# Kernel tuning notes

Measured on AMD Instinct MI355X. Metric: run time of the kernel, lower is better.

## Reference

```python
import jax, jax.numpy as jnp
import numpy as np

B, T, C = 4, 2048, 2048
D_ATT, D_FFN = 2048, 8192
EPS = 1e-5

def setup_inputs() -> dict:
    key = jax.random.key(0)
    ks = jax.random.split(key, 20)
    n = lambda k, s, sc=0.02: jax.random.normal(k, s, dtype=jnp.float32) * sc
    u = lambda k, s: jax.random.uniform(k, s, dtype=jnp.float32)
    return {
        'x': jax.random.normal(ks[0], (B, T, C), dtype=jnp.float32),
        'ln1_w': jnp.ones((C,), jnp.float32), 'ln1_b': jnp.zeros((C,), jnp.float32),
        'ln2_w': jnp.ones((C,), jnp.float32), 'ln2_b': jnp.zeros((C,), jnp.float32),
        'tm_k': u(ks[1], (1, 1, C)), 'tm_v': u(ks[2], (1, 1, C)), 'tm_r': u(ks[3], (1, 1, C)),
        'time_decay': n(ks[4], (D_ATT,), 1.0),            # raw; decay = -exp(time_decay)
        'time_first': n(ks[5], (D_ATT,), 0.3) + float(np.log(0.3)),
        'Wk': n(ks[6], (D_ATT, C)), 'Wv': n(ks[7], (D_ATT, C)),
        'Wr': n(ks[8], (D_ATT, C)), 'Wo': n(ks[9], (C, D_ATT)),
        'cm_k': u(ks[10], (1, 1, C)), 'cm_r': u(ks[11], (1, 1, C)),
        'Wck': n(ks[12], (D_FFN, C)), 'Wcv': n(ks[13], (C, D_FFN)), 'Wcr': n(ks[14], (C, C)),
    }

def layer_norm(x, w, b):
    mu = jnp.mean(x, axis=-1, keepdims=True)
    var = jnp.var(x, axis=-1, keepdims=True)
    return (x - mu) * jax.lax.rsqrt(var + EPS) * w + b

def time_shift(x):
    # xx[:, t] = x[:, t-1], zero at t=0
    return jnp.pad(x, ((0, 0), (1, 0), (0, 0)))[:, :-1]

def wkv(time_decay, time_first, k, v):
    # Numerically-stable WKV linear recurrence (RWKV-4). k, v: [B,T,D]
    decay = -jnp.exp(time_decay)  # [D]
    kT = jnp.swapaxes(k, 0, 1)    # [T,B,D]
    vT = jnp.swapaxes(v, 0, 1)

    def step(carry, kv_t):
        aa, bb, pp = carry
        kt, vt = kv_t
        ww = time_first + kt
        p = jnp.maximum(pp, ww)
        e1 = jnp.exp(pp - p)
        e2 = jnp.exp(ww - p)
        out = (e1 * aa + e2 * vt) / (e1 * bb + e2)
        ww2 = pp + decay
        p2 = jnp.maximum(ww2, kt)
        e1b = jnp.exp(ww2 - p2)
        e2b = jnp.exp(kt - p2)
        return (e1b * aa + e2b * vt, e1b * bb + e2b, p2), out

    z = jnp.zeros((k.shape[0], k.shape[2]), k.dtype)
    init = (z, z, jnp.full_like(z, -1e38))
    _, outT = jax.lax.scan(step, init, (kT, vT))
    return jnp.swapaxes(outT, 0, 1)  # [B,T,D]

def reference(x, ln1_w, ln1_b, ln2_w, ln2_b, tm_k, tm_v, tm_r,
              time_decay, time_first, Wk, Wv, Wr, Wo,
              cm_k, cm_r, Wck, Wcv, Wcr):
    # --- TimeMix ---
    h = layer_norm(x, ln1_w, ln1_b)
    hh = time_shift(h)
    xk = h * tm_k + hh * (1 - tm_k)
    xv = h * tm_v + hh * (1 - tm_v)
    xr = h * tm_r + hh * (1 - tm_r)
    k = jnp.einsum('btc,dc->btd', xk, Wk)
    v = jnp.einsum('btc,dc->btd', xv, Wv)
    sr = jax.nn.sigmoid(jnp.einsum('btc,dc->btd', xr, Wr))
    rwkv = sr * wkv(time_decay, time_first, k, v)
    x = x + jnp.einsum('btd,cd->btc', rwkv, Wo)
    # --- ChannelMix ---
    g = layer_norm(x, ln2_w, ln2_b)
    gg = time_shift(g)
    xk2 = g * cm_k + gg * (1 - cm_k)
    xr2 = g * cm_r + gg * (1 - cm_r)
    kf = jnp.square(jax.nn.relu(jnp.einsum('btc,fc->btf', xk2, Wck)))
    kv = jnp.einsum('btf,cf->btc', kf, Wcv)
    x = x + jax.nn.sigmoid(jnp.einsum('btc,dc->btd', xr2, Wcr)) * kv
    return x
```

## Files before the change

kernel.cpp:

```cpp
#include <hip/hip_runtime.h>
#include <hip/hip_bf16.h>

#define B_ 4
#define T_ 2048
#define C_ 2048
#define D_ 2048
#define F_ 8192
#define BT_ (B_*T_)
#define NCH 64
#define LCH 32

using bf16 = __hip_bfloat16;
typedef __attribute__((ext_vector_type(8))) short bf16x8;
typedef __attribute__((ext_vector_type(4))) float f32x4;

template<bool V> struct BC { static constexpr bool value = V; };

struct bf4 { bf16 a, b, c, d; };

__device__ __forceinline__ bf4 to_bf4(float x, float y, float z, float w) {
  bf4 r;
  r.a = __float2bfloat16(x); r.b = __float2bfloat16(y);
  r.c = __float2bfloat16(z); r.d = __float2bfloat16(w);
  return r;
}

__device__ __forceinline__ void cvt_body(const float* __restrict__ in,
                                         bf16* __restrict__ out,
                                         int i, int stride, int n4) {
  for (; i < n4; i += stride) {
    float4 v = ((const float4*)in)[i];
    ((bf4*)out)[i] = to_bf4(v.x, v.y, v.z, v.w);
  }
}

__device__ __forceinline__ void block_reduce4(float v[4], float out[4]) {
  #pragma unroll
  for (int i = 0; i < 4; ++i)
    #pragma unroll
    for (int off = 1; off < 64; off <<= 1)
      v[i] += __shfl_xor(v[i], off);
  __shared__ float red[4][4];
  int wave = threadIdx.x >> 6, lane = threadIdx.x & 63;
  if (lane == 0) {
    red[wave][0] = v[0]; red[wave][1] = v[1];
    red[wave][2] = v[2]; red[wave][3] = v[3];
  }
  __syncthreads();
  #pragma unroll
  for (int i = 0; i < 4; ++i)
    out[i] = red[0][i] + red[1][i] + red[2][i] + red[3][i];
}

__global__ __launch_bounds__(256) void mixcvt1_kernel(
    const float* __restrict__ x, const float* __restrict__ w, const float* __restrict__ b,
    const float* __restrict__ tmk, const float* __restrict__ tmv, const float* __restrict__ tmr,
    bf16* __restrict__ xk, bf16* __restrict__ xv, bf16* __restrict__ xr,
    const float* __restrict__ W0, const float* __restrict__ W1,
    const float* __restrict__ W2, const float* __restrict__ W3,
    bf16* __restrict__ o0, bf16* __restrict__ o1,
    bf16* __restrict__ o2, bf16* __restrict__ o3) {
  if (blockIdx.x >= BT_) {
    const int lb4 = blockIdx.x - BT_;
    const int sub = lb4 >> 10;
    const int lb = lb4 & 1023;
    const float* in = (sub == 0) ? W0 : (sub == 1) ? W1 : (sub == 2) ? W2 : W3;
    bf16* o = (sub == 0) ? o0 : (sub == 1) ? o1 : (sub == 2) ? o2 : o3;
    cvt_body(in, o, lb * 256 + threadIdx.x, 1024 * 256, D_ * C_ / 4);
    return;
  }
  const int row = blockIdx.x;
  const int t = row & (T_ - 1);
  const bool hasPrev = (t != 0);
  const int tid = threadIdx.x;
  const float* xc = x + (size_t)row * C_;
  const float* xp = xc - C_;
  float c[8], p[8];
  *(float4*)&c[0] = *(const float4*)(xc + tid * 4);
  *(float4*)&c[4] = *(const float4*)(xc + tid * 4 + 1024);
  if (hasPrev) {
    *(float4*)&p[0] = *(const float4*)(xp + tid * 4);
    *(float4*)&p[4] = *(const float4*)(xp + tid * 4 + 1024);
  } else {
    #pragma unroll
    for (int j = 0; j < 8; ++j) p[j] = 0.f;
  }
  float v[4] = {0.f, 0.f, 0.f, 0.f}, tot[4];
  #pragma unroll
  for (int j = 0; j < 8; ++j) {
    v[0] += c[j]; v[1] += c[j] * c[j];
    v[2] += p[j]; v[3] += p[j] * p[j];
  }
  block_reduce4(v, tot);
  const float muc = tot[0] * (1.f / C_);
  const float rsc = rsqrtf(tot[1] * (1.f / C_) - muc * muc + 1e-5f);
  const float mup = tot[2] * (1.f / C_);
  const float rsp = rsqrtf(tot[3] * (1.f / C_) - mup * mup + 1e-5f);
  float wv[8], bv[8], mk[8], mv[8], mr[8];
  #pragma unroll
  for (int half = 0; half < 2; ++half) {
    int i = tid * 4 + half * 1024;
    *(float4*)&wv[half*4] = *(const float4*)(w + i);
    *(float4*)&bv[half*4] = *(const float4*)(b + i);
    *(float4*)&mk[half*4] = *(const float4*)(tmk + i);
    *(float4*)&mv[half*4] = *(const float4*)(tmv + i);
    *(float4*)&mr[half*4] = *(const float4*)(tmr + i);
  }
  float ok[8], ov[8], orr[8];
  #pragma unroll
  for (int j = 0; j < 8; ++j) {
    float h  = (c[j] - muc) * rsc * wv[j] + bv[j];
    float hh = hasPrev ? ((p[j] - mup) * rsp * wv[j] + bv[j]) : 0.f;
    ok[j]  = hh + mk[j] * (h - hh);
    ov[j]  = hh + mv[j] * (h - hh);
    orr[j] = hh + mr[j] * (h - hh);
  }
  size_t ro = (size_t)row * C_;
  #pragma unroll
  for (int half = 0; half < 2; ++half) {
    int i = tid * 4 + half * 1024;
    *(bf4*)(xk + ro + i) = to_bf4(ok[half*4], ok[half*4+1], ok[half*4+2], ok[half*4+3]);
    *(bf4*)(xv + ro + i) = to_bf4(ov[half*4], ov[half*4+1], ov[half*4+2], ov[half*4+3]);
    *(bf4*)(xr + ro + i) = to_bf4(orr[half*4], orr[half*4+1], orr[half*4+2], orr[half*4+3]);
  }
}

__global__ __launch_bounds__(256) void mixcvt2_kernel(
    const float* __restrict__ x, const float* __restrict__ w, const float* __restrict__ b,
    const float* __restrict__ cmk, const float* __restrict__ cmr,
    bf16* __restrict__ xk2, bf16* __restrict__ xr2,
    const float* __restrict__ Wcr, bf16* __restrict__ Wcr_b,
    const float* __restrict__ Wck, bf16* __restrict__ Wck_b) {
  if (blockIdx.x >= BT_) {
    const int lb = blockIdx.x - BT_;
    if (lb < 512)
      cvt_body(Wcr, Wcr_b, lb * 256 + threadIdx.x, 512 * 256, C_ * C_ / 4);
    else
      cvt_body(Wck, Wck_b, (lb - 512) * 256 + threadIdx.x, 2048 * 256, F_ * C_ / 4);
    return;
  }
  const int row = blockIdx.x;
  const int t = row & (T_ - 1);
  const bool hasPrev = (t != 0);
  const int tid = threadIdx.x;
  const float* xc = x + (size_t)row * C_;
  const float* xp = xc - C_;
  float c[8], p[8];
  *(float4*)&c[0] = *(const float4*)(xc + tid * 4);
  *(float4*)&c[4] = *(const float4*)(xc + tid * 4 + 1024);
  if (hasPrev) {
    *(float4*)&p[0] = *(const float4*)(xp + tid * 4);
    *(float4*)&p[4] = *(const float4*)(xp + tid * 4 + 1024);
  } else {
    #pragma unroll
    for (int j = 0; j < 8; ++j) p[j] = 0.f;
  }
  float v[4] = {0.f, 0.f, 0.f, 0.f}, tot[4];
  #pragma unroll
  for (int j = 0; j < 8; ++j) {
    v[0] += c[j]; v[1] += c[j] * c[j];
    v[2] += p[j]; v[3] += p[j] * p[j];
  }
  block_reduce4(v, tot);
  const float muc = tot[0] * (1.f / C_);
  const float rsc = rsqrtf(tot[1] * (1.f / C_) - muc * muc + 1e-5f);
  const float mup = tot[2] * (1.f / C_);
  const float rsp = rsqrtf(tot[3] * (1.f / C_) - mup * mup + 1e-5f);
  float wv[8], bv[8], mk[8], mr[8];
  #pragma unroll
  for (int half = 0; half < 2; ++half) {
    int i = tid * 4 + half * 1024;
    *(float4*)&wv[half*4] = *(const float4*)(w + i);
    *(float4*)&bv[half*4] = *(const float4*)(b + i);
    *(float4*)&mk[half*4] = *(const float4*)(cmk + i);
    *(float4*)&mr[half*4] = *(const float4*)(cmr + i);
  }
  float ok[8], orr[8];
  #pragma unroll
  for (int j = 0; j < 8; ++j) {
    float h  = (c[j] - muc) * rsc * wv[j] + bv[j];
    float hh = hasPrev ? ((p[j] - mup) * rsp * wv[j] + bv[j]) : 0.f;
    ok[j]  = hh + mk[j] * (h - hh);
    orr[j] = hh + mr[j] * (h - hh);
  }
  size_t ro = (size_t)row * C_;
  #pragma unroll
  for (int half = 0; half < 2; ++half) {
    int i = tid * 4 + half * 1024;
    *(bf4*)(xk2 + ro + i) = to_bf4(ok[half*4], ok[half*4+1], ok[half*4+2], ok[half*4+3]);
    *(bf4*)(xr2 + ro + i) = to_bf4(orr[half*4], orr[half*4+1], orr[half*4+2], orr[half*4+3]);
  }
}

__global__ __launch_bounds__(256) void wkv_pass1(
    const bf16* __restrict__ kp, const bf16* __restrict__ vp,
    const float* __restrict__ td,
    float* __restrict__ sA, float* __restrict__ sB, float* __restrict__ sP) {
  const int g = blockIdx.x * 256 + threadIdx.x;
  const int d = g & (D_ - 1);
  const int c = (g >> 11) & (NCH - 1);
  const int b = g >> 17;
  const float w = -__expf(td[d]);
  const size_t base = ((size_t)b * T_ + c * LCH) * D_ + d;
  float aa = 0.f, bb = 0.f, pp = -1e38f;
  #pragma unroll 4
  for (int j = 0; j < LCH; ++j) {
    float kt = __bfloat162float(kp[base + (size_t)j * D_]);
    float vt = __bfloat162float(vp[base + (size_t)j * D_]);
    float ww2 = pp + w;
    float p2 = fmaxf(ww2, kt);
    float e1 = __expf(ww2 - p2), e2 = __expf(kt - p2);
    aa = e1 * aa + e2 * vt;
    bb = e1 * bb + e2;
    pp = p2;
  }
  const int sidx = ((b * NCH + c) << 11) + d;
  sA[sidx] = aa; sB[sidx] = bb; sP[sidx] = pp;
}

__global__ __launch_bounds__(256) void wkv_pass2(
    const float* __restrict__ td,
    float* __restrict__ sA, float* __restrict__ sB, float* __restrict__ sP) {
  const int g = blockIdx.x * 256 + threadIdx.x;
  const int d = g & (D_ - 1);
  const int b = g >> 11;
  const float wL = -__expf(td[d]) * (float)LCH;
  float aa = 0.f, bb = 0.f, pp = -1e38f;
  for (int c = 0; c < NCH; ++c) {
    const int sidx = ((b * NCH + c) << 11) + d;
    float la = sA[sidx], lb = sB[sidx], lp = sP[sidx];
    sA[sidx] = aa; sB[sidx] = bb; sP[sidx] = pp;
    float ww2 = pp + wL;
    float q = fmaxf(ww2, lp);
    float e1 = __expf(ww2 - q), e2 = __expf(lp - q);
    aa = e1 * aa + e2 * la;
    bb = e1 * bb + e2 * lb;
    pp = q;
  }
}

__global__ __launch_bounds__(256) void wkv_pass3(
    const bf16* __restrict__ kp, const bf16* __restrict__ vp, const bf16* __restrict__ rp,
    const float* __restrict__ td, const float* __restrict__ tfp,
    const float* __restrict__ sA, const float* __restrict__ sB, const float* __restrict__ sP,
    bf16* __restrict__ rwkv) {
  const int g = blockIdx.x * 256 + threadIdx.x;
  const int d = g & (D_ - 1);
  const int c = (g >> 11) & (NCH - 1);
  const int b = g >> 17;
  const float w = -__expf(td[d]);
  const float u = tfp[d];
  const int sidx = ((b * NCH + c) << 11) + d;
  float aa = sA[sidx], bb = sB[sidx], pp = sP[sidx];
  const size_t base = ((size_t)b * T_ + c * LCH) * D_ + d;
  #pragma unroll 4
  for (int j = 0; j < LCH; ++j) {
    float kt = __bfloat162float(kp[base + (size_t)j * D_]);
    float vt = __bfloat162float(vp[base + (size_t)j * D_]);
    float rt = __bfloat162float(rp[base + (size_t)j * D_]);
    float ww = u + kt;
    float p = fmaxf(pp, ww);
    float e1 = __expf(pp - p);
    float e2 = __expf(ww - p);
    float outv = (e1 * aa + e2 * vt) / (e1 * bb + e2);
    float sr = 1.f / (1.f + __expf(-rt));
    rwkv[base + (size_t)j * D_] = __float2bfloat16(sr * outv);
    float ww2 = pp + w;
    float p2 = fmaxf(ww2, kt);
    float e1b = __expf(ww2 - p2);
    float e2b = __expf(kt - p2);
    aa = e1b * aa + e2b * vt;
    bb = e1b * bb + e2b;
    pp = p2;
  }
}

template<int EPI>
__device__ __forceinline__ void gemm_core(
    const bf16* __restrict__ A, const bf16* __restrict__ Bt,
    int N, int K, int id, int nwg,
    float* __restrict__ outF, bf16* __restrict__ outB,
    const float* __restrict__ addP, const bf16* __restrict__ sigP,
    char* lds) {
  const int tid = threadIdx.x;
  const int wid = tid >> 6, lane = tid & 63;
  const int wm = wid >> 2, wn = wid & 3;

  const int cpx = nwg >> 3;
  const int sid = (id & 7) * cpx + (id >> 3);
  const int nx = N >> 8;
  const int band = sid / (4 * nx);
  const int rem = sid - band * (4 * nx);
  const int bx = rem >> 2;
  const int by = band * 4 + (rem & 3);
  const int tileM = by * 256, tileN = bx * 256;

  const int NT = K >> 6;

  const int srow_lo = wid * 8 + (lane >> 3);
  const int scel = ((lane & 7) ^ (lane >> 3)) << 3;

  const bf16* pA[2][2];
  const bf16* pB[2][2];
  #pragma unroll
  for (int h = 0; h < 2; ++h)
    #pragma unroll
    for (int j = 0; j < 2; ++j) {
      pA[h][j] = A  + (size_t)(tileM + h * 128 + srow_lo + j * 64) * K + scel;
      pB[h][j] = Bt + (size_t)(tileN + h * 128 + srow_lo + j * 64) * K + scel;
    }
  const int ldsW = wid * 1024;

  auto stA = [&](int par, int h, int eo) {
    #pragma unroll
    for (int j = 0; j < 2; ++j)
      __builtin_amdgcn_global_load_lds(
          (const __attribute__((address_space(1))) void*)(pA[h][j] + eo),
          (__attribute__((address_space(3))) void*)(lds + par * 32768 + h * 16384 + j * 8192 + ldsW),
          16, 0, 0);
  };
  auto stB = [&](int par, int h, int eo) {
    #pragma unroll
    for (int j = 0; j < 2; ++j)
      __builtin_amdgcn_global_load_lds(
          (const __attribute__((address_space(1))) void*)(pB[h][j] + eo),
          (__attribute__((address_space(3))) void*)(lds + 65536 + par * 32768 + h * 16384 + j * 8192 + ldsW),
          16, 0, 0);
  };

  const int lane15 = lane & 15;
  const int kswz0 = ((lane >> 4) * 16) ^ ((lane & 7) << 4);
  const int aBase = (wm * 128 + lane15) * 128;
  const int bBase = (wn * 64 + lane15) * 128;

  f32x4 acc[8][4] = {};

  stB(0, 0, 0); stB(0, 1, 0); stA(0, 0, 0); stA(0, 1, 0); stB(1, 0, 64); stB(1, 1, 64);
  asm volatile("s_waitcnt vmcnt(4)" : : : "memory");
  __builtin_amdgcn_s_barrier();
  __builtin_amdgcn_sched_barrier(0);

  auto tileBody = [&](int par, auto doa, auto dob, int aEo, int bEo) {
    constexpr bool DOA = decltype(doa)::value;
    constexpr bool DOB = decltype(dob)::value;
    const char* Ab = lds + (par << 15);
    const char* Bb = lds + 65536 + (par << 15);
    bf16x8 bfr[4][2];
    #pragma unroll
    for (int q = 0; q < 4; ++q) {
      if (q == 0) {
        #pragma unroll
        for (int n = 0; n < 4; ++n) {
          bfr[n][0] = *(const bf16x8*)(Bb + bBase + n * 2048 + kswz0);
          bfr[n][1] = *(const bf16x8*)(Bb + bBase + n * 2048 + (kswz0 ^ 64));
        }
      }
      bf16x8 am[2][2];
      #pragma unroll
      for (int mm = 0; mm < 2; ++mm) {
        am[mm][0] = *(const bf16x8*)(Ab + aBase + q * 4096 + mm * 2048 + kswz0);
        am[mm][1] = *(const bf16x8*)(Ab + aBase + q * 4096 + mm * 2048 + (kswz0 ^ 64));
      }
      if constexpr (DOA) {
        if (q == 0) stA(par ^ 1, 0, aEo);
        if (q == 1) stA(par ^ 1, 1, aEo);
      }
      if constexpr (DOB) {
        if (q == 2) stB(par, 0, bEo);
        if (q == 3) stB(par, 1, bEo);
      }
      if (q == 0)
        asm volatile("s_waitcnt lgkmcnt(8)" : : : "memory");
      __builtin_amdgcn_sched_barrier(0);
      __builtin_amdgcn_s_barrier();
      __builtin_amdgcn_sched_barrier(0);
      __builtin_amdgcn_s_setprio(1);
      #pragma unroll
      for (int kk = 0; kk < 2; ++kk)
        #pragma unroll
        for (int n = 0; n < 4; ++n) {
          acc[2*q+0][n] = __builtin_amdgcn_mfma_f32_16x16x32_bf16(am[0][kk], bfr[n][kk], acc[2*q+0][n], 0, 0, 0);
          acc[2*q+1][n] = __builtin_amdgcn_mfma_f32_16x16x32_bf16(am[1][kk], bfr[n][kk], acc[2*q+1][n], 0, 0, 0);
        }
      __builtin_amdgcn_s_setprio(0);
      __builtin_amdgcn_sched_barrier(0);
      if (q == 3) {
        if constexpr (DOB)      asm volatile("s_waitcnt vmcnt(4)" : : : "memory");
        else if constexpr (DOA) asm volatile("s_waitcnt vmcnt(0)" : : : "memory");
      }
      __builtin_amdgcn_s_barrier();
      __builtin_amdgcn_sched_barrier(0);
    }
  };

  for (int t = 0; t < NT - 2; t += 2) {
    tileBody(0, BC<true>{}, BC<true>{}, 64, 128);
    tileBody(1, BC<true>{}, BC<true>{}, 128, 192);
    #pragma unroll
    for (int h = 0; h < 2; ++h)
      #pragma unroll
      for (int j = 0; j < 2; ++j) { pA[h][j] += 128; pB[h][j] += 128; }
  }
  tileBody(0, BC<true>{}, BC<false>{}, 64, 0);
  tileBody(1, BC<false>{}, BC<false>{}, 0, 0);

  const int erow0 = tileM + wm * 128 + (lane >> 4) * 4;
  const int ecol0 = tileN + wn * 64 + lane15;
  #pragma unroll
  for (int m = 0; m < 8; ++m) {
    #pragma unroll
    for (int n = 0; n < 4; ++n) {
      #pragma unroll
      for (int r = 0; r < 4; ++r) {
        const int grow = erow0 + m * 16 + r;
        const int gcol = ecol0 + n * 16;
        const size_t idx = (size_t)grow * N + gcol;
        const float val = acc[m][n][r];
        if constexpr (EPI == 0) {
          outB[idx] = __float2bfloat16(val);
        } else if constexpr (EPI == 1) {
          float tt = fmaxf(val, 0.f);
          outB[idx] = __float2bfloat16(tt * tt);
        } else if constexpr (EPI == 2) {
          outF[idx] = addP[idx] + val;
        } else if constexpr (EPI == 3) {
          outB[idx] = __float2bfloat16(1.f / (1.f + __expf(-val)));
        } else {
          outF[idx] = addP[idx] + __bfloat162float(sigP[idx]) * val;
        }
      }
    }
  }
}

template<int EPI>
__global__ __launch_bounds__(512, 2) void gemm256(
    const bf16* __restrict__ A, const bf16* __restrict__ Bt,
    int N, int K,
    float* __restrict__ outF, bf16* __restrict__ outB,
    const float* __restrict__ addP, const bf16* __restrict__ sigP) {
  __shared__ alignas(16) char lds[131072];
  gemm_core<EPI>(A, Bt, N, K, blockIdx.x, gridDim.x, outF, outB, addP, sigP, lds);
}

__global__ __launch_bounds__(512, 2) void gemm_kvr(
    const bf16* __restrict__ A0, const bf16* __restrict__ A1, const bf16* __restrict__ A2,
    const bf16* __restrict__ B0, const bf16* __restrict__ B1, const bf16* __restrict__ B2,
    bf16* __restrict__ O0, bf16* __restrict__ O1, bf16* __restrict__ O2) {
  __shared__ alignas(16) char lds[131072];
  const int sub = blockIdx.x >> 8;
  const int bid = blockIdx.x & 255;
  const bf16* A  = (sub == 0) ? A0 : (sub == 1) ? A1 : A2;
  const bf16* Bt = (sub == 0) ? B0 : (sub == 1) ? B1 : B2;
  bf16* O        = (sub == 0) ? O0 : (sub == 1) ? O1 : O2;
  gemm_core<0>(A, Bt, D_, C_, bid, 256, nullptr, O, nullptr, nullptr, lds);
}

__global__ __launch_bounds__(512, 2) void gemm_kf_cvt(
    const bf16* __restrict__ A, const bf16* __restrict__ Bt, bf16* __restrict__ kf,
    const float* __restrict__ Wcv, bf16* __restrict__ Wcv_b) {
  __shared__ alignas(16) char lds[131072];
  if (blockIdx.x < 512) {
    cvt_body(Wcv, Wcv_b, blockIdx.x * 512 + threadIdx.x, 512 * 512, C_ * F_ / 4);
    return;
  }
  gemm_core<1>(A, Bt, F_, C_, blockIdx.x - 512, 1024, nullptr, kf, nullptr, nullptr, lds);
}

extern "C" void kernel_launch(void* const* d_in, const int* in_sizes, int n_in,
                              void* d_out, int out_size, void* d_ws, size_t ws_size,
                              hipStream_t stream) {
  const float* x    = (const float*)d_in[0];
  const float* ln1w = (const float*)d_in[1];
  const float* ln1b = (const float*)d_in[2];
  const float* ln2w = (const float*)d_in[3];
  const float* ln2b = (const float*)d_in[4];
  const float* tmk  = (const float*)d_in[5];
  const float* tmv  = (const float*)d_in[6];
  const float* tmr  = (const float*)d_in[7];
  const float* td   = (const float*)d_in[8];
  const float* tf   = (const float*)d_in[9];
  const float* Wk   = (const float*)d_in[10];
  const float* Wv   = (const float*)d_in[11];
  const float* Wr   = (const float*)d_in[12];
  const float* Wo   = (const float*)d_in[13];
  const float* cmk  = (const float*)d_in[14];
  const float* cmr  = (const float*)d_in[15];
  const float* Wck  = (const float*)d_in[16];
  const float* Wcv  = (const float*)d_in[17];
  const float* Wcr  = (const float*)d_in[18];
  float* out = (float*)d_out;

  char* ws = (char*)d_ws;
  const size_t MB = 1ull << 20;
  bf16* R0 = (bf16*)(ws + 0 * MB);
  bf16* R1 = (bf16*)(ws + 32 * MB);
  bf16* R2 = (bf16*)(ws + 64 * MB);
  bf16* R3 = (bf16*)(ws + 96 * MB);
  bf16* R4 = (bf16*)(ws + 128 * MB);

  bf16* xk = R1, *xv = R2, *xr = R3;
  bf16* k_ = R4;
  bf16* v_ = (bf16*)(ws + 160 * MB);
  bf16* r_ = (bf16*)(ws + 192 * MB);
  bf16* rwkv = R1;

  bf16* xk2 = R1, *xr2 = R2, *sig = R3, *kf = R4;
  bf16* Wcr_b = R4;
  bf16* Wck_b = R0;
  bf16* Wcv_b = R2;

  bf16* Wk_b = R0;
  bf16* Wv_b = R0 + (size_t)D_ * C_;
  bf16* Wr_b = R0 + (size_t)2 * D_ * C_;
  bf16* Wo_b = R0 + (size_t)3 * D_ * C_;

  float* sA = (float*)R0;
  float* sB = sA + (size_t)B_ * NCH * D_;
  float* sP = sB + (size_t)B_ * NCH * D_;

  const int gN2k = (BT_ / 256) * (D_ / 256);

  mixcvt1_kernel<<<BT_ + 4096, 256, 0, stream>>>(x, ln1w, ln1b, tmk, tmv, tmr,
      xk, xv, xr, Wk, Wv, Wr, Wo, Wk_b, Wv_b, Wr_b, Wo_b);
  gemm_kvr<<<768, 512, 0, stream>>>(xk, xv, xr, Wk_b, Wv_b, Wr_b, k_, v_, r_);
  wkv_pass1<<<B_ * NCH * D_ / 256, 256, 0, stream>>>(k_, v_, td, sA, sB, sP);
  wkv_pass2<<<B_ * D_ / 256, 256, 0, stream>>>(td, sA, sB, sP);
  wkv_pass3<<<B_ * NCH * D_ / 256, 256, 0, stream>>>(k_, v_, r_, td, tf, sA, sB, sP, rwkv);
  gemm256<2><<<gN2k, 512, 0, stream>>>(rwkv, Wo_b, C_, D_, out, nullptr, x, nullptr);

  mixcvt2_kernel<<<BT_ + 2560, 256, 0, stream>>>(out, ln2w, ln2b, cmk, cmr,
      xk2, xr2, Wcr, Wcr_b, Wck, Wck_b);
  gemm256<3><<<gN2k, 512, 0, stream>>>(xr2, Wcr_b, C_, C_, nullptr, sig, nullptr, nullptr);
  gemm_kf_cvt<<<1536, 512, 0, stream>>>(xk2, Wck_b, kf, Wcv, Wcv_b);
  gemm256<4><<<gN2k, 512, 0, stream>>>(kf, Wcv_b, C_, F_, out, nullptr, out, sig);
}
```

Measured before the change: 923.9 us.

## Parallelize WKV chunk combine with warp scan and overlap weight casts with GEMMs

```diff
diff --git a/kernel.cpp b/kernel.cpp
--- a/kernel.cpp
+++ b/kernel.cpp
@@ -125,20 +125,10 @@
   }
 }
 
-__global__ __launch_bounds__(256) void mixcvt2_kernel(
+__global__ __launch_bounds__(256) void mix2_kernel(
     const float* __restrict__ x, const float* __restrict__ w, const float* __restrict__ b,
     const float* __restrict__ cmk, const float* __restrict__ cmr,
-    bf16* __restrict__ xk2, bf16* __restrict__ xr2,
-    const float* __restrict__ Wcr, bf16* __restrict__ Wcr_b,
-    const float* __restrict__ Wck, bf16* __restrict__ Wck_b) {
-  if (blockIdx.x >= BT_) {
-    const int lb = blockIdx.x - BT_;
-    if (lb < 512)
-      cvt_body(Wcr, Wcr_b, lb * 256 + threadIdx.x, 512 * 256, C_ * C_ / 4);
-    else
-      cvt_body(Wck, Wck_b, (lb - 512) * 256 + threadIdx.x, 2048 * 256, F_ * C_ / 4);
-    return;
-  }
+    bf16* __restrict__ xk2, bf16* __restrict__ xr2) {
   const int row = blockIdx.x;
   const int t = row & (T_ - 1);
   const bool hasPrev = (t != 0);
@@ -221,22 +211,30 @@
 __global__ __launch_bounds__(256) void wkv_pass2(
     const float* __restrict__ td,
     float* __restrict__ sA, float* __restrict__ sB, float* __restrict__ sP) {
-  const int g = blockIdx.x * 256 + threadIdx.x;
-  const int d = g & (D_ - 1);
-  const int b = g >> 11;
+  const int wv = blockIdx.x * 4 + (threadIdx.x >> 6);
+  const int lane = threadIdx.x & 63;
+  const int d = wv & (D_ - 1);
+  const int b = wv >> 11;
   const float wL = -__expf(td[d]) * (float)LCH;
-  float aa = 0.f, bb = 0.f, pp = -1e38f;
-  for (int c = 0; c < NCH; ++c) {
-    const int sidx = ((b * NCH + c) << 11) + d;
-    float la = sA[sidx], lb = sB[sidx], lp = sP[sidx];
-    sA[sidx] = aa; sB[sidx] = bb; sP[sidx] = pp;
-    float ww2 = pp + wL;
-    float q = fmaxf(ww2, lp);
-    float e1 = __expf(ww2 - q), e2 = __expf(lp - q);
-    aa = e1 * aa + e2 * la;
-    bb = e1 * bb + e2 * lb;
-    pp = q;
-  }
+  const int sidx = ((b * NCH + lane) << 11) + d;
+  float aa = sA[sidx], bb = sB[sidx], pp = sP[sidx];
+  #pragma unroll
+  for (int s = 1; s < 64; s <<= 1) {
+    float la = __shfl_up(aa, s);
+    float lb = __shfl_up(bb, s);
+    float lp = __shfl_up(pp, s);
+    if (lane >= s) {
+      float lpd = lp + wL * (float)s;
+      float q = fmaxf(lpd, pp);
+      float e1 = __expf(lpd - q), e2 = __expf(pp - q);
+      aa = e1 * la + e2 * aa;
+      bb = e1 * lb + e2 * bb;
+      pp = q;
+    }
+  }
+  float ea = __shfl_up(aa, 1), eb = __shfl_up(bb, 1), ep = __shfl_up(pp, 1);
+  if (lane == 0) { ea = 0.f; eb = 0.f; ep = -1e38f; }
+  sA[sidx] = ea; sB[sidx] = eb; sP[sidx] = ep;
 }
 
 __global__ __launch_bounds__(256) void wkv_pass3(
@@ -456,6 +454,29 @@
   gemm_core<0>(A, Bt, D_, C_, bid, 256, nullptr, O, nullptr, nullptr, lds);
 }
 
+__global__ __launch_bounds__(512, 2) void gemm_wo_cvt(
+    const bf16* __restrict__ rwkv, const bf16* __restrict__ Wo_b,
+    float* __restrict__ out, const float* __restrict__ x,
+    const float* __restrict__ Wcr, bf16* __restrict__ Wcr_b) {
+  __shared__ alignas(16) char lds[131072];
+  if (blockIdx.x >= 256) {
+    cvt_body(Wcr, Wcr_b, (blockIdx.x - 256) * 512 + threadIdx.x, 512 * 512, C_ * C_ / 4);
+    return;
+  }
+  gemm_core<2>(rwkv, Wo_b, C_, D_, blockIdx.x, 256, out, nullptr, x, nullptr, lds);
+}
+
+__global__ __launch_bounds__(512, 2) void gemm_sig_cvt(
+    const bf16* __restrict__ xr2, const bf16* __restrict__ Wcr_b, bf16* __restrict__ sig,
+    const float* __restrict__ Wck, bf16* __restrict__ Wck_b) {
+  __shared__ alignas(16) char lds[131072];
+  if (blockIdx.x >= 256) {
+    cvt_body(Wck, Wck_b, (blockIdx.x - 256) * 512 + threadIdx.x, 1024 * 512, F_ * C_ / 4);
+    return;
+  }
+  gemm_core<3>(xr2, Wcr_b, C_, C_, blockIdx.x, 256, nullptr, sig, nullptr, nullptr, lds);
+}
+
 __global__ __launch_bounds__(512, 2) void gemm_kf_cvt(
     const bf16* __restrict__ A, const bf16* __restrict__ Bt, bf16* __restrict__ kf,
     const float* __restrict__ Wcv, bf16* __restrict__ Wcv_b) {
@@ -525,13 +546,12 @@
       xk, xv, xr, Wk, Wv, Wr, Wo, Wk_b, Wv_b, Wr_b, Wo_b);
   gemm_kvr<<<768, 512, 0, stream>>>(xk, xv, xr, Wk_b, Wv_b, Wr_b, k_, v_, r_);
   wkv_pass1<<<B_ * NCH * D_ / 256, 256, 0, stream>>>(k_, v_, td, sA, sB, sP);
-  wkv_pass2<<<B_ * D_ / 256, 256, 0, stream>>>(td, sA, sB, sP);
+  wkv_pass2<<<B_ * D_ / 4, 256, 0, stream>>>(td, sA, sB, sP);
   wkv_pass3<<<B_ * NCH * D_ / 256, 256, 0, stream>>>(k_, v_, r_, td, tf, sA, sB, sP, rwkv);
-  gemm256<2><<<gN2k, 512, 0, stream>>>(rwkv, Wo_b, C_, D_, out, nullptr, x, nullptr);
-
-  mixcvt2_kernel<<<BT_ + 2560, 256, 0, stream>>>(out, ln2w, ln2b, cmk, cmr,
-      xk2, xr2, Wcr, Wcr_b, Wck, Wck_b);
-  gemm256<3><<<gN2k, 512, 0, stream>>>(xr2, Wcr_b, C_, C_, nullptr, sig, nullptr, nullptr);
+  gemm_wo_cvt<<<768, 512, 0, stream>>>(rwkv, Wo_b, out, x, Wcr, Wcr_b);
+
+  mix2_kernel<<<BT_, 256, 0, stream>>>(out, ln2w, ln2b, cmk, cmr, xk2, xr2);
+  gemm_sig_cvt<<<1280, 512, 0, stream>>>(xr2, Wcr_b, sig, Wck, Wck_b);
   gemm_kf_cvt<<<1536, 512, 0, stream>>>(xk2, Wck_b, kf, Wcv, Wcv_b);
   gemm256<4><<<gN2k, 512, 0, stream>>>(kf, Wcv_b, C_, F_, out, nullptr, out, sig);
 }
```

Result: slower. 944.5 us (+2.2%).
